# Kernel tuning notes

Hardware: AMD Instinct MI355X
Metric: run time of the kernel (lower is better)

The kernel has to match this reference:

```python
import jax, jax.numpy as jnp
import numpy as np

# ---- static hyperparams (from comp_encoding.__init__ / DMPNNEncoderLayer) ----
B = 512            # number of molecules in the batch (wrapper's python loop)
A = 128            # padded atoms per molecule == max_mol_len
E = 256            # padded directed bonds per molecule
K = 6              # max incoming bonds gathered per bond/atom
ATOM_FDIM = 133
BOND_FDIM = 14
H = 128            # d_hidden = max_mol_len
DEPTH = 3
G = 2048           # global feature dim (Morgan fingerprint)


def _mol_lens():
    ml = np.array(jax.random.randint(jax.random.fold_in(jax.random.key(0), 5), (B,), 16, H + 1))
    ml[0] = H  # ensure comp_dim == max(mol_lens) == H so per-row padding is a no-op
    return ml


def setup_inputs() -> dict:
    key = jax.random.key(0)
    ks = jax.random.split(key, 10)
    atom_feature = jax.random.normal(ks[0], (B, A, ATOM_FDIM), jnp.float32)
    f_ini_atoms_bond = jax.random.normal(ks[1], (B, E, ATOM_FDIM + BOND_FDIM), jnp.float32)
    atom_to_incoming_bond = jax.random.randint(ks[2], (B, A, K), 0, E)
    mapping = jax.random.randint(ks[3], (B, E, K), 0, E)
    global_f = jax.random.normal(ks[4], (B, G), jnp.float32)
    mol_lens = _mol_lens()  # static numpy ints (constants, drive output shapes)
    W_i = jax.random.normal(ks[6], (H, ATOM_FDIM + BOND_FDIM), jnp.float32) / np.float32(np.sqrt(ATOM_FDIM + BOND_FDIM))
    W_h = jax.random.normal(ks[7], (H, H), jnp.float32) / np.float32(np.sqrt(H))
    W_o = jax.random.normal(ks[8], (H, ATOM_FDIM + H), jnp.float32) / np.float32(np.sqrt(ATOM_FDIM + H))
    b_o = jax.random.normal(ks[9], (H,), jnp.float32) * 0.01
    return dict(atom_feature=atom_feature, f_ini_atoms_bond=f_ini_atoms_bond,
                atom_to_incoming_bond=atom_to_incoming_bond, mapping=mapping,
                global_f=global_f, mol_lens=mol_lens,
                W_i=W_i, W_h=W_h, W_o=W_o, b_o=b_o)


def _gather_sum(msg, idx):
    # msg: [B, E, H]; idx: [B, N, K] -> sum over K incoming messages: [B, N, H]
    b, n, k = idx.shape
    g = jnp.take_along_axis(msg, idx.reshape(b, n * k)[..., None], axis=1)
    return g.reshape(b, n, k, -1).sum(axis=2)


def reference(atom_feature, f_ini_atoms_bond, atom_to_incoming_bond, mapping,
              global_f, mol_lens, W_i, W_h, W_o, b_o):
    # DMPNN: W_i on initial directed-bond features
    inp = jnp.einsum('bef,hf->beh', f_ini_atoms_bond, W_i)   # [B, E, H]
    msg = jax.nn.relu(inp)
    for _ in range(DEPTH - 1):
        agg = _gather_sum(msg, mapping)                      # [B, E, H]
        msg = jax.nn.relu(inp + jnp.einsum('beh,gh->beg', agg, W_h))
    m2a = _gather_sum(msg, atom_to_incoming_bond)            # [B, A, H]
    cat = jnp.concatenate([atom_feature, m2a], axis=-1)      # [B, A, 133+H]
    atoms_h = jax.nn.relu(jnp.einsum('bad,hd->bah', cat, W_o) + b_o)  # [B, A, H]

    # wrapper: take first mol_len atom encodings per molecule, stack, build mask
    ml = np.asarray(mol_lens)
    valid = np.arange(A)[None, :] < ml[:, None]              # [B, A] static
    b_idx, a_idx = np.nonzero(valid)
    comp = atoms_h[b_idx, a_idx]                             # [sum(mol_lens), H]
    c_mask = jnp.asarray(valid.astype(np.float32))           # [B, comp_dim]
    return comp, c_mask
```

## Files before the change

kernel.cpp:

```cpp
#include <hip/hip_runtime.h>
#include <hip/hip_bf16.h>

typedef unsigned int   uint;
typedef unsigned short ushort;
typedef short bf16x8 __attribute__((ext_vector_type(8)));
typedef float f32x4  __attribute__((ext_vector_type(4)));

constexpr int Bm   = 512;
constexpr int Aa   = 128;
constexpr int Ee   = 256;
constexpr int Kk   = 6;
constexpr int AFD  = 133;
constexpr int FD   = 147;
constexpr int Hh   = 128;
constexpr int CATD = 261;
constexpr int KWI  = 192;
constexpr int KWO  = 320;

__device__ __forceinline__ int msg_idx(int row, int col) {
    return row * 128 + (col ^ ((row & 7) << 3));
}

__device__ __forceinline__ ushort f2b(float f) {
    uint u = __float_as_uint(f);
    u += 0x7FFFu + ((u >> 16) & 1u);
    return (ushort)(u >> 16);
}
__device__ __forceinline__ uint cvt2(float x, float y) {
    float2 t2; t2.x = x; t2.y = y;
    __hip_bfloat162 t = __float22bfloat162_rn(t2);
    uint r; __builtin_memcpy(&r, &t, 4); return r;
}
__device__ __forceinline__ float2 b2f2(uint p) {
    float2 r;
    r.x = __uint_as_float(p << 16);
    r.y = __uint_as_float(p & 0xFFFF0000u);
    return r;
}

__device__ __forceinline__ bf16x8 gsum6(const ushort* src, const int* mr, int ko) {
    float2 s0 = {0.f, 0.f}, s1 = {0.f, 0.f}, s2 = {0.f, 0.f}, s3 = {0.f, 0.f};
#pragma unroll
    for (int k = 0; k < Kk; ++k) {
        const int sw = (mr[k] >> 4) & 56;
        uint4 m = *(const uint4*)&src[mr[k] + (ko ^ sw)];
        float2 a = b2f2(m.x); s0.x += a.x; s0.y += a.y;
        float2 b = b2f2(m.y); s1.x += b.x; s1.y += b.y;
        float2 d = b2f2(m.z); s2.x += d.x; s2.y += d.y;
        float2 e = b2f2(m.w); s3.x += e.x; s3.y += e.y;
    }
    uint4 o;
    o.x = cvt2(s0.x, s0.y); o.y = cvt2(s1.x, s1.y);
    o.z = cvt2(s2.x, s2.y); o.w = cvt2(s3.x, s3.y);
    bf16x8 r;
    __builtin_memcpy(&r, &o, 16);
    return r;
}

__device__ __forceinline__ bf16x8 ld_frag_f32(const float* sp, int c0, int lim) {
    float v[8];
#pragma unroll
    for (int d = 0; d < 8; ++d) v[d] = (c0 + d < lim) ? sp[d] : 0.f;
    uint4 o;
    o.x = cvt2(v[0], v[1]); o.y = cvt2(v[2], v[3]);
    o.z = cvt2(v[4], v[5]); o.w = cvt2(v[6], v[7]);
    bf16x8 r;
    __builtin_memcpy(&r, &o, 16);
    return r;
}

__global__ __launch_bounds__(256) void k_prep_w(const float* __restrict__ Wi,
                                                const float* __restrict__ Wh,
                                                const float* __restrict__ Wo,
                                                ushort* __restrict__ Wi_b,
                                                ushort* __restrict__ Wh_b,
                                                ushort* __restrict__ Wo_b) {
    const int h = blockIdx.x, t = threadIdx.x;
    for (int c = t; c < KWI; c += 256)
        Wi_b[h * KWI + c] = f2b(c < FD ? Wi[h * FD + c] : 0.f);
    for (int c = t; c < Hh; c += 256)
        Wh_b[h * Hh + c] = f2b(Wh[h * Hh + c]);
    for (int c = t; c < KWO; c += 256) {
        float v = 0.f;
        if (c < AFD)       v = Wo[h * CATD + c];
        else if (c >= 192) v = Wo[h * CATD + AFD + (c - 192)];
        Wo_b[h * KWO + c] = f2b(v);
    }
}

__global__ __launch_bounds__(512) void k_scan(const int* __restrict__ ml,
                                              int* __restrict__ pfx) {
    __shared__ int s[512];
    int t = threadIdx.x;
    s[t] = ml[t];
    __syncthreads();
    for (int off = 1; off < 512; off <<= 1) {
        int v = (t >= off) ? s[t - off] : 0;
        __syncthreads();
        s[t] += v;
        __syncthreads();
    }
    pfx[t + 1] = s[t];
    if (t == 0) pfx[0] = 0;
}

__global__ __launch_bounds__(512, 2) void k_fused(
        const float* __restrict__ atomf,
        const float* __restrict__ fini,
        const int*   __restrict__ a2ib,
        const int*   __restrict__ mapping,
        const ushort* __restrict__ Wi_b,
        const ushort* __restrict__ Wh_b,
        const ushort* __restrict__ Wo_b,
        const float* __restrict__ bo,
        const int*   __restrict__ mol_lens,
        const int*   __restrict__ pfx,
        float* __restrict__ out,
        float* __restrict__ cmask) {
    __shared__ ushort msg[Ee * 128];

    const int b    = blockIdx.x;
    const int tid  = threadIdx.x;
    const int wave = tid >> 6;
    const int lane = tid & 63;
    const int l15  = lane & 15, quad = lane >> 4;

    const int len = mol_lens[b];
    if (tid < Aa) cmask[b * Aa + tid] = (tid < len) ? 1.0f : 0.0f;

    int mr[2][Kk];
#pragma unroll
    for (int i = 0; i < 2; ++i) {
        const int row = wave * 32 + i * 16 + l15;
        const int* mp = &mapping[((size_t)b * Ee + row) * Kk];
#pragma unroll
        for (int k = 0; k < Kk; ++k) mr[i][k] = mp[k] * 128;
    }

    f32x4 acc[2][8];
#pragma unroll
    for (int i = 0; i < 2; ++i)
#pragma unroll
        for (int j = 0; j < 8; ++j) acc[i][j] = (f32x4){0.f, 0.f, 0.f, 0.f};

    const float* fsrc = fini + (size_t)b * Ee * FD;
#pragma unroll
    for (int c = 0; c < 3; ++c) {
#pragma unroll
        for (int ks = 0; ks < 2; ++ks) {
            const int c0 = c * 64 + ks * 32 + quad * 8;
            bf16x8 af[2];
#pragma unroll
            for (int i = 0; i < 2; ++i) {
                const int row = wave * 32 + i * 16 + l15;
                af[i] = ld_frag_f32(fsrc + (size_t)row * FD + c0, c0, FD);
            }
#pragma unroll
            for (int jh = 0; jh < 2; ++jh) {
                bf16x8 bf[4];
#pragma unroll
                for (int j = 0; j < 4; ++j)
                    bf[j] = *(const bf16x8*)&Wi_b[((jh * 4 + j) * 16 + l15) * KWI + c0];
#pragma unroll
                for (int i = 0; i < 2; ++i)
#pragma unroll
                    for (int j = 0; j < 4; ++j)
                        acc[i][jh * 4 + j] = __builtin_amdgcn_mfma_f32_16x16x32_bf16(
                            af[i], bf[j], acc[i][jh * 4 + j], 0, 0, 0);
            }
        }
    }

    uint2 inp_pk[2][8];
#pragma unroll
    for (int i = 0; i < 2; ++i)
#pragma unroll
        for (int j = 0; j < 8; ++j) {
            f32x4 a4 = acc[i][j];
            uint2 p;
            p.x = cvt2(a4[0], a4[1]);
            p.y = cvt2(a4[2], a4[3]);
            inp_pk[i][j] = p;
            const int col = j * 16 + l15;
#pragma unroll
            for (int reg = 0; reg < 4; ++reg) {
                const int row = wave * 32 + i * 16 + quad * 4 + reg;
                float v = a4[reg] > 0.f ? a4[reg] : 0.f;
                msg[msg_idx(row, col)] = f2b(v);
            }
        }
    __syncthreads();

#pragma unroll
    for (int h = 0; h < 2; ++h) {
#pragma unroll
        for (int i = 0; i < 2; ++i)
#pragma unroll
            for (int j = 0; j < 8; ++j) {
                float2 lo = b2f2(inp_pk[i][j].x);
                float2 hi = b2f2(inp_pk[i][j].y);
                acc[i][j] = (f32x4){lo.x, lo.y, hi.x, hi.y};
            }
#pragma unroll
        for (int ks = 0; ks < 4; ++ks) {
            const int ko = ks * 32 + quad * 8;
            bf16x8 af[2];
#pragma unroll
            for (int i = 0; i < 2; ++i) af[i] = gsum6(msg, mr[i], ko);
#pragma unroll
            for (int jh = 0; jh < 2; ++jh) {
                bf16x8 bf[4];
#pragma unroll
                for (int j = 0; j < 4; ++j)
                    bf[j] = *(const bf16x8*)&Wh_b[((jh * 4 + j) * 16 + l15) * Hh + ko];
#pragma unroll
                for (int i = 0; i < 2; ++i)
#pragma unroll
                    for (int j = 0; j < 4; ++j)
                        acc[i][jh * 4 + j] = __builtin_amdgcn_mfma_f32_16x16x32_bf16(
                            af[i], bf[j], acc[i][jh * 4 + j], 0, 0, 0);
            }
        }
        __syncthreads();
#pragma unroll
        for (int i = 0; i < 2; ++i)
#pragma unroll
            for (int j = 0; j < 8; ++j) {
                const int col = j * 16 + l15;
#pragma unroll
                for (int reg = 0; reg < 4; ++reg) {
                    const int row = wave * 32 + i * 16 + quad * 4 + reg;
                    float v = acc[i][j][reg];
                    msg[msg_idx(row, col)] = f2b(v > 0.f ? v : 0.f);
                }
            }
        __syncthreads();
    }

    f32x4 ro[8];
#pragma unroll
    for (int j = 0; j < 8; ++j) ro[j] = (f32x4){0.f, 0.f, 0.f, 0.f};

    const int arow = wave * 16 + l15;

    {
        int ar[Kk];
        const int* ap = &a2ib[((size_t)b * Aa + arow) * Kk];
#pragma unroll
        for (int k = 0; k < Kk; ++k) ar[k] = ap[k] * 128;
#pragma unroll
        for (int ks = 0; ks < 4; ++ks) {
            const int ko = ks * 32 + quad * 8;
            bf16x8 a0 = gsum6(msg, ar, ko);
#pragma unroll
            for (int jh = 0; jh < 2; ++jh) {
                bf16x8 bf[4];
#pragma unroll
                for (int j = 0; j < 4; ++j)
                    bf[j] = *(const bf16x8*)&Wo_b[((jh * 4 + j) * 16 + l15) * KWO + 192 + ko];
#pragma unroll
                for (int j = 0; j < 4; ++j)
                    ro[jh * 4 + j] = __builtin_amdgcn_mfma_f32_16x16x32_bf16(
                        a0, bf[j], ro[jh * 4 + j], 0, 0, 0);
            }
        }
    }

    const float* asrc = atomf + (size_t)b * Aa * AFD;
#pragma unroll
    for (int c = 0; c < 3; ++c) {
#pragma unroll
        for (int ks = 0; ks < 2; ++ks) {
            const int c0 = c * 64 + ks * 32 + quad * 8;
            bf16x8 a0 = ld_frag_f32(asrc + (size_t)arow * AFD + c0, c0, AFD);
#pragma unroll
            for (int jh = 0; jh < 2; ++jh) {
                bf16x8 bf[4];
#pragma unroll
                for (int j = 0; j < 4; ++j)
                    bf[j] = *(const bf16x8*)&Wo_b[((jh * 4 + j) * 16 + l15) * KWO + c0];
#pragma unroll
                for (int j = 0; j < 4; ++j)
                    ro[jh * 4 + j] = __builtin_amdgcn_mfma_f32_16x16x32_bf16(
                        a0, bf[j], ro[jh * 4 + j], 0, 0, 0);
            }
        }
    }

    const int base = pfx[b];
#pragma unroll
    for (int j = 0; j < 8; ++j) {
        const int col = j * 16 + l15;
        const float bv = bo[col];
#pragma unroll
        for (int reg = 0; reg < 4; ++reg) {
            const int a = wave * 16 + quad * 4 + reg;
            if (a < len) {
                float v = ro[j][reg] + bv;
                out[(size_t)(base + a) * Hh + col] = v > 0.f ? v : 0.f;
            }
        }
    }
}

extern "C" void kernel_launch(void* const* d_in, const int* in_sizes, int n_in,
                              void* d_out, int out_size, void* d_ws, size_t ws_size,
                              hipStream_t stream) {
    const float* atom_feature = (const float*)d_in[0];
    const float* f_ini        = (const float*)d_in[1];
    const int*   a2ib         = (const int*)d_in[2];
    const int*   mapping      = (const int*)d_in[3];
    const int*   mol_lens     = (const int*)d_in[5];
    const float* Wi           = (const float*)d_in[6];
    const float* Wh           = (const float*)d_in[7];
    const float* Wo           = (const float*)d_in[8];
    const float* bo           = (const float*)d_in[9];
    float* out = (float*)d_out;

    ushort* Wi_b = (ushort*)d_ws;
    ushort* Wh_b = Wi_b + 128 * KWI;
    ushort* Wo_b = Wh_b + 128 * Hh;
    int*    pfx  = (int*)(Wo_b + 128 * KWO);

    float* cmask = out + ((size_t)out_size - (size_t)Bm * Aa);

    k_prep_w<<<128, 256, 0, stream>>>(Wi, Wh, Wo, Wi_b, Wh_b, Wo_b);
    k_scan  <<<1, 512, 0, stream>>>(mol_lens, pfx);
    k_fused <<<Bm, 512, 0, stream>>>(atom_feature, f_ini, a2ib, mapping,
                                     Wi_b, Wh_b, Wo_b, bo, mol_lens, pfx,
                                     out, cmask);
}
```

Baseline: 297.4 us.

## Stage bond features and index tables in LDS, double-buffer messages with padded rows

Bond features are now loaded with coalesced 16-byte global reads, converted to bf16 and staged in shared memory in two halves before the W_i MFMA. Previously each lane read its own strided fp32 row fragment. The gather index tables also move into shared memory. The XOR swizzle is replaced by row padding (stride 136), and ping-pong msg0/msg1 buffers remove one barrier per depth step. The K loop shrinks from 6 to 5 steps of 32 because only 147 or 133 columns are needed. The cost is much larger LDS use (about 150 KB), which with 512-thread blocks likely leaves one block per CU instead of the declared two, lowering occupancy.

Result: slower. 308.5 us (+3.8%).

```diff
diff --git a/kernel.cpp b/kernel.cpp
--- a/kernel.cpp
+++ b/kernel.cpp
@@ -16,10 +16,8 @@
 constexpr int CATD = 261;
 constexpr int KWI  = 192;
 constexpr int KWO  = 320;
-
-__device__ __forceinline__ int msg_idx(int row, int col) {
-    return row * 128 + (col ^ ((row & 7) << 3));
-}
+constexpr int MST  = 136;
+constexpr int FST  = 152;
 
 __device__ __forceinline__ ushort f2b(float f) {
     uint u = __float_as_uint(f);
@@ -42,8 +40,7 @@
     float2 s0 = {0.f, 0.f}, s1 = {0.f, 0.f}, s2 = {0.f, 0.f}, s3 = {0.f, 0.f};
 #pragma unroll
     for (int k = 0; k < Kk; ++k) {
-        const int sw = (mr[k] >> 4) & 56;
-        uint4 m = *(const uint4*)&src[mr[k] + (ko ^ sw)];
+        uint4 m = *(const uint4*)&src[mr[k] + ko];
         float2 a = b2f2(m.x); s0.x += a.x; s0.y += a.y;
         float2 b = b2f2(m.y); s1.x += b.x; s1.y += b.y;
         float2 d = b2f2(m.z); s2.x += d.x; s2.y += d.y;
@@ -117,7 +114,10 @@
         const int*   __restrict__ pfx,
         float* __restrict__ out,
         float* __restrict__ cmask) {
-    __shared__ ushort msg[Ee * 128];
+    __shared__ ushort msg0[Ee * MST];
+    __shared__ ushort msg1[Ee * MST];
+    __shared__ int    map_s[Ee * Kk];
+    __shared__ int    a2_s[Aa * Kk];
 
     const int b    = blockIdx.x;
     const int tid  = threadIdx.x;
@@ -125,36 +125,41 @@
     const int lane = tid & 63;
     const int l15  = lane & 15, quad = lane >> 4;
 
+    for (int i = tid; i < Ee * Kk; i += 512) map_s[i] = mapping[b * Ee * Kk + i];
+    for (int i = tid; i < Aa * Kk; i += 512) a2_s[i]  = a2ib[b * Aa * Kk + i];
+    if (tid < 8) msg1[128 * FST + tid] = 0;
     const int len = mol_lens[b];
     if (tid < Aa) cmask[b * Aa + tid] = (tid < len) ? 1.0f : 0.0f;
 
-    int mr[2][Kk];
-#pragma unroll
-    for (int i = 0; i < 2; ++i) {
-        const int row = wave * 32 + i * 16 + l15;
-        const int* mp = &mapping[((size_t)b * Ee + row) * Kk];
-#pragma unroll
-        for (int k = 0; k < Kk; ++k) mr[i][k] = mp[k] * 128;
-    }
-
-    f32x4 acc[2][8];
-#pragma unroll
-    for (int i = 0; i < 2; ++i)
-#pragma unroll
-        for (int j = 0; j < 8; ++j) acc[i][j] = (f32x4){0.f, 0.f, 0.f, 0.f};
-
-    const float* fsrc = fini + (size_t)b * Ee * FD;
-#pragma unroll
-    for (int c = 0; c < 3; ++c) {
-#pragma unroll
-        for (int ks = 0; ks < 2; ++ks) {
-            const int c0 = c * 64 + ks * 32 + quad * 8;
-            bf16x8 af[2];
-#pragma unroll
-            for (int i = 0; i < 2; ++i) {
-                const int row = wave * 32 + i * 16 + l15;
-                af[i] = ld_frag_f32(fsrc + (size_t)row * FD + c0, c0, FD);
-            }
+    uint2 inp_pk[2][8];
+
+#pragma unroll
+    for (int half = 0; half < 2; ++half) {
+        const uint4* fsrc4 = (const uint4*)(fini + (size_t)b * Ee * FD) + half * 4704;
+        for (int k = tid; k < 4704; k += 512) {
+            uint4 q = fsrc4[k];
+            const int d0 = half * 18816 + k * 4;
+#pragma unroll
+            for (int i = 0; i < 4; ++i) {
+                const int d = d0 + i;
+                const int r = d / FD;
+                uint w = (i == 0) ? q.x : (i == 1) ? q.y : (i == 2) ? q.z : q.w;
+                msg1[d + 5 * r - half * 19456] = f2b(__uint_as_float(w));
+            }
+        }
+        for (int i = tid; i < 128 * 5; i += 512) {
+            const int r = i / 5, c = FD + (i - r * 5);
+            msg1[r * FST + c] = 0;
+        }
+        __syncthreads();
+
+        f32x4 acc[8];
+#pragma unroll
+        for (int j = 0; j < 8; ++j) acc[j] = (f32x4){0.f, 0.f, 0.f, 0.f};
+#pragma unroll
+        for (int ks = 0; ks < 5; ++ks) {
+            const int c0 = ks * 32 + quad * 8;
+            bf16x8 af = *(const bf16x8*)&msg1[(wave * 16 + l15) * FST + c0];
 #pragma unroll
             for (int jh = 0; jh < 2; ++jh) {
                 bf16x8 bf[4];
@@ -162,96 +167,90 @@
                 for (int j = 0; j < 4; ++j)
                     bf[j] = *(const bf16x8*)&Wi_b[((jh * 4 + j) * 16 + l15) * KWI + c0];
 #pragma unroll
-                for (int i = 0; i < 2; ++i)
-#pragma unroll
-                    for (int j = 0; j < 4; ++j)
-                        acc[i][jh * 4 + j] = __builtin_amdgcn_mfma_f32_16x16x32_bf16(
-                            af[i], bf[j], acc[i][jh * 4 + j], 0, 0, 0);
-            }
-        }
-    }
-
-    uint2 inp_pk[2][8];
-#pragma unroll
-    for (int i = 0; i < 2; ++i)
+                for (int j = 0; j < 4; ++j)
+                    acc[jh * 4 + j] = __builtin_amdgcn_mfma_f32_16x16x32_bf16(
+                        af, bf[j], acc[jh * 4 + j], 0, 0, 0);
+            }
+        }
 #pragma unroll
         for (int j = 0; j < 8; ++j) {
-            f32x4 a4 = acc[i][j];
+            f32x4 a4 = acc[j];
             uint2 p;
             p.x = cvt2(a4[0], a4[1]);
             p.y = cvt2(a4[2], a4[3]);
-            inp_pk[i][j] = p;
+            inp_pk[half][j] = p;
             const int col = j * 16 + l15;
 #pragma unroll
             for (int reg = 0; reg < 4; ++reg) {
-                const int row = wave * 32 + i * 16 + quad * 4 + reg;
+                const int row = half * 128 + wave * 16 + quad * 4 + reg;
                 float v = a4[reg] > 0.f ? a4[reg] : 0.f;
-                msg[msg_idx(row, col)] = f2b(v);
-            }
-        }
-    __syncthreads();
+                msg0[row * MST + col] = f2b(v);
+            }
+        }
+        __syncthreads();
+    }
 
 #pragma unroll
     for (int h = 0; h < 2; ++h) {
-#pragma unroll
-        for (int i = 0; i < 2; ++i)
+        const ushort* src = h ? msg1 : msg0;
+        ushort*       dst = h ? msg0 : msg1;
+#pragma unroll
+        for (int i = 0; i < 2; ++i) {
+            const int rowA = i * 128 + wave * 16 + l15;
+            int mr[Kk];
+#pragma unroll
+            for (int k = 0; k < Kk; ++k) mr[k] = map_s[rowA * Kk + k] * MST;
+            f32x4 acc[8];
 #pragma unroll
             for (int j = 0; j < 8; ++j) {
                 float2 lo = b2f2(inp_pk[i][j].x);
                 float2 hi = b2f2(inp_pk[i][j].y);
-                acc[i][j] = (f32x4){lo.x, lo.y, hi.x, hi.y};
-            }
+                acc[j] = (f32x4){lo.x, lo.y, hi.x, hi.y};
+            }
+#pragma unroll
+            for (int ks = 0; ks < 4; ++ks) {
+                const int ko = ks * 32 + quad * 8;
+                bf16x8 af = gsum6(src, mr, ko);
+#pragma unroll
+                for (int jh = 0; jh < 2; ++jh) {
+                    bf16x8 bf[4];
+#pragma unroll
+                    for (int j = 0; j < 4; ++j)
+                        bf[j] = *(const bf16x8*)&Wh_b[((jh * 4 + j) * 16 + l15) * Hh + ko];
+#pragma unroll
+                    for (int j = 0; j < 4; ++j)
+                        acc[jh * 4 + j] = __builtin_amdgcn_mfma_f32_16x16x32_bf16(
+                            af, bf[j], acc[jh * 4 + j], 0, 0, 0);
+                }
+            }
+#pragma unroll
+            for (int j = 0; j < 8; ++j) {
+                const int col = j * 16 + l15;
+#pragma unroll
+                for (int reg = 0; reg < 4; ++reg) {
+                    const int row = i * 128 + wave * 16 + quad * 4 + reg;
+                    float v = acc[j][reg];
+                    dst[row * MST + col] = f2b(v > 0.f ? v : 0.f);
+                }
+            }
+        }
+        __syncthreads();
+    }
+
+    f32x4 ro[8];
+#pragma unroll
+    for (int j = 0; j < 8; ++j) ro[j] = (f32x4){0.f, 0.f, 0.f, 0.f};
+
+    const int arow = wave * 16 + l15;
+
+    {
+        int ar[Kk];
+#pragma unroll
+        for (int k = 0; k < Kk; ++k) ar[k] = a2_s[arow * Kk + k] * MST;
 #pragma unroll
         for (int ks = 0; ks < 4; ++ks) {
             const int ko = ks * 32 + quad * 8;
-            bf16x8 af[2];
-#pragma unroll
-            for (int i = 0; i < 2; ++i) af[i] = gsum6(msg, mr[i], ko);
-#pragma unroll
-            for (int jh = 0; jh < 2; ++jh) {
-                bf16x8 bf[4];
-#pragma unroll
-                for (int j = 0; j < 4; ++j)
-                    bf[j] = *(const bf16x8*)&Wh_b[((jh * 4 + j) * 16 + l15) * Hh + ko];
-#pragma unroll
-                for (int i = 0; i < 2; ++i)
-#pragma unroll
-                    for (int j = 0; j < 4; ++j)
-                        acc[i][jh * 4 + j] = __builtin_amdgcn_mfma_f32_16x16x32_bf16(
-                            af[i], bf[j], acc[i][jh * 4 + j], 0, 0, 0);
-            }
-        }
-        __syncthreads();
-#pragma unroll
-        for (int i = 0; i < 2; ++i)
-#pragma unroll
-            for (int j = 0; j < 8; ++j) {
-                const int col = j * 16 + l15;
-#pragma unroll
-                for (int reg = 0; reg < 4; ++reg) {
-                    const int row = wave * 32 + i * 16 + quad * 4 + reg;
-                    float v = acc[i][j][reg];
-                    msg[msg_idx(row, col)] = f2b(v > 0.f ? v : 0.f);
-                }
-            }
-        __syncthreads();
-    }
-
-    f32x4 ro[8];
-#pragma unroll
-    for (int j = 0; j < 8; ++j) ro[j] = (f32x4){0.f, 0.f, 0.f, 0.f};
-
-    const int arow = wave * 16 + l15;
-
-    {
-        int ar[Kk];
-        const int* ap = &a2ib[((size_t)b * Aa + arow) * Kk];
-#pragma unroll
-        for (int k = 0; k < Kk; ++k) ar[k] = ap[k] * 128;
-#pragma unroll
-        for (int ks = 0; ks < 4; ++ks) {
-            const int ko = ks * 32 + quad * 8;
-            bf16x8 a0 = gsum6(msg, ar, ko);
+            bf16x8 a0 = gsum6(msg0, ar, ko);
 #pragma unroll
             for (int jh = 0; jh < 2; ++jh) {
                 bf16x8 bf[4];
@@ -268,22 +267,19 @@
 
     const float* asrc = atomf + (size_t)b * Aa * AFD;
 #pragma unroll
-    for (int c = 0; c < 3; ++c) {
-#pragma unroll
-        for (int ks = 0; ks < 2; ++ks) {
-            const int c0 = c * 64 + ks * 32 + quad * 8;
-            bf16x8 a0 = ld_frag_f32(asrc + (size_t)arow * AFD + c0, c0, AFD);
-#pragma unroll
-            for (int jh = 0; jh < 2; ++jh) {
-                bf16x8 bf[4];
-#pragma unroll
-                for (int j = 0; j < 4; ++j)
-                    bf[j] = *(const bf16x8*)&Wo_b[((jh * 4 + j) * 16 + l15) * KWO + c0];
-#pragma unroll
-                for (int j = 0; j < 4; ++j)
-                    ro[jh * 4 + j] = __builtin_amdgcn_mfma_f32_16x16x32_bf16(
-                        a0, bf[j], ro[jh * 4 + j], 0, 0, 0);
-            }
+    for (int ksi = 0; ksi < 5; ++ksi) {
+        const int c0 = ksi * 32 + quad * 8;
+        bf16x8 a0 = ld_frag_f32(asrc + (size_t)arow * AFD + c0, c0, AFD);
+#pragma unroll
+        for (int jh = 0; jh < 2; ++jh) {
+            bf16x8 bf[4];
+#pragma unroll
+            for (int j = 0; j < 4; ++j)
+                bf[j] = *(const bf16x8*)&Wo_b[((jh * 4 + j) * 16 + l15) * KWO + c0];
+#pragma unroll
+            for (int j = 0; j < 4; ++j)
+                ro[jh * 4 + j] = __builtin_amdgcn_mfma_f32_16x16x32_bf16(
+                    a0, bf[j], ro[jh * 4 + j], 0, 0, 0);
         }
     }
 
```
